# Kernel tuning notes

Measured on AMD Instinct MI355X. Metric: run time of the kernel, lower is better.

## Reference

```python
import jax, jax.numpy as jnp
import numpy as np

EMBED_DIM = 1024
NUM_HEADS = 16
PROJ_DIM = EMBED_DIM // NUM_HEADS


def setup_inputs() -> dict:
    key = jax.random.key(0)
    ks = jax.random.split(key, 11)
    B, S, D = 2, 2048, EMBED_DIM
    scale = 1.0 / np.sqrt(D)
    inp = {
        'q': jax.random.normal(ks[0], (B, S, D), jnp.float32),
        'k': jax.random.normal(ks[1], (B, S, D), jnp.float32),
        'v': jax.random.normal(ks[2], (B, S, D), jnp.float32),
        'Wq': jax.random.normal(ks[3], (D, D), jnp.float32) * scale,
        'bq': jnp.zeros((D,), jnp.float32),
        'Wk': jax.random.normal(ks[4], (D, D), jnp.float32) * scale,
        'bk': jnp.zeros((D,), jnp.float32),
        'Wv': jax.random.normal(ks[5], (D, D), jnp.float32) * scale,
        'bv': jnp.zeros((D,), jnp.float32),
        'Wo': jax.random.normal(ks[6], (D, D), jnp.float32) * scale,
        'bo': jnp.zeros((D,), jnp.float32),
        'use_causal_mask': 1,
    }
    return inp


def _split_heads(x, B):
    # [B, S, D] -> [B, H, S, Pd]
    return x.reshape(B, -1, NUM_HEADS, PROJ_DIM).transpose(0, 2, 1, 3)


def reference(q, k, v, Wq, bq, Wk, bk, Wv, bv, Wo, bo, use_causal_mask):
    B, S, D = q.shape
    qh = _split_heads(q @ Wq + bq, B)
    kh = _split_heads(k @ Wk + bk, B)
    vh = _split_heads(v @ Wv + bv, B)
    # scaled dot-product attention; scores [B, H, S, S]
    logits = jnp.einsum('bhqd,bhkd->bhqk', qh, kh) / jnp.sqrt(
        jnp.asarray(PROJ_DIM, jnp.float32))
    if use_causal_mask:
        # faithful to source: logits += log(tril * 1e-9 + 1e-9)
        tril = jnp.tril(jnp.ones((S, S), dtype=logits.dtype))
        logits = logits + jnp.log(tril * 1e-9 + 1e-9)
    attn = jax.nn.softmax(logits, axis=-1)
    out = jnp.einsum('bhqk,bhkd->bhqd', attn, vh)
    out = out.transpose(0, 2, 1, 3).reshape(B, S, D)
    return out @ Wo + bo
```

## Files before the change

kernel.cpp:

```cpp
#include <hip/hip_runtime.h>
#include <hip/hip_bf16.h>
#include <stdint.h>

#define EMBED 1024
#define NH    16
#define PD    64
#define BATCH 2
#define SEQ   2048

typedef unsigned short u16;
typedef __attribute__((ext_vector_type(8))) short bf16x8;
typedef __attribute__((ext_vector_type(4))) float f32x4;

#define WAITALL() __builtin_amdgcn_s_waitcnt(0)

__device__ __forceinline__ float b2f(u16 x) {
  unsigned u = ((unsigned)x) << 16;
  return __builtin_bit_cast(float, u);
}
__device__ __forceinline__ u16 cvtb(float x) {
  __bf16 h = (__bf16)x;
  return __builtin_bit_cast(u16, h);
}
__device__ __forceinline__ float loadIn(const void* p, size_t i, int isf32) {
  return isf32 ? ((const float*)p)[i] : b2f(((const u16*)p)[i]);
}
__device__ __forceinline__ void async16(const void* g, void* l) {
  __builtin_amdgcn_global_load_lds((const __attribute__((address_space(1))) void*)g,
                                   (__attribute__((address_space(3))) void*)l,
                                   16, 0, 0);
}
__device__ __forceinline__ int detect_f32(const void* q) {
  unsigned w0 = ((const unsigned*)q)[threadIdx.x & 63];
  unsigned e = (w0 >> 7) & 0xffu;
  unsigned long long m = __ballot(e >= 110 && e <= 135);
  return (__popcll(m) < 32) ? 1 : 0;
}

__global__ __launch_bounds__(256) void conv_fused(
    const void* q, const void* k, const void* v,
    const void* Wq, const void* Wk, const void* Wv, const void* Wo,
    u16* qb, u16* kb, u16* vb, u16* WT_all) {
  __shared__ float sh[64][65];
  const int isf32 = detect_f32(q);

  if (blockIdx.y < 3) {
    size_t i = ((size_t)blockIdx.x * 256 + threadIdx.x) * 8;
    const void* src = (blockIdx.y == 0) ? q : (blockIdx.y == 1) ? k : v;
    u16* dst = (blockIdx.y == 0) ? qb : (blockIdx.y == 1) ? kb : vb;
    u16 tmp[8];
    if (isf32) {
      const float* s = (const float*)src + i;
      float4 a = *(const float4*)s;
      float4 b = *(const float4*)(s + 4);
      tmp[0] = cvtb(a.x); tmp[1] = cvtb(a.y); tmp[2] = cvtb(a.z); tmp[3] = cvtb(a.w);
      tmp[4] = cvtb(b.x); tmp[5] = cvtb(b.y); tmp[6] = cvtb(b.z); tmp[7] = cvtb(b.w);
    } else {
      const uint4 r = *(const uint4*)((const u16*)src + i);
      *(uint4*)tmp = r;
    }
    *(uint4*)(dst + i) = *(uint4*)tmp;
    return;
  }

  if (blockIdx.x >= 1024) return;
  const int z = blockIdx.x >> 8;
  const int xy = blockIdx.x & 255;
  const int bx = xy & 15, by = xy >> 4;
  const void* W = (z == 0) ? Wq : (z == 1) ? Wk : (z == 2) ? Wv : Wo;
  u16* WT = WT_all + (size_t)z * EMBED * EMBED;
  int r0 = by * 64, c0 = bx * 64;
  int col = threadIdx.x & 63;
  int rb  = threadIdx.x >> 6;
#pragma unroll
  for (int i = 0; i < 16; i++) {
    int row = i * 4 + rb;
    sh[row][col] = loadIn(W, (size_t)(r0 + row) * EMBED + c0 + col, isf32);
  }
  __syncthreads();
#pragma unroll
  for (int i = 0; i < 16; i++) {
    int row = i * 4 + rb;
    WT[(size_t)(c0 + row) * EMBED + r0 + col] = cvtb(sh[col][row]);
  }
}

__device__ __forceinline__ void gemm_stage(const u16* __restrict__ A,
                                           const u16* __restrict__ Bt,
                                           int tm, int tn, int kt,
                                           u16* As, u16* Bs, int tid) {
#pragma unroll
  for (int i = 0; i < 4; i++) {
    int c = i * 256 + tid;
    int row = c >> 3;
    int col = ((c & 7) << 3) ^ ((row & 7) << 3);
    async16(A + (size_t)(tm + row) * EMBED + kt + col, As + c * 8);
    async16(Bt + (size_t)(tn + row) * EMBED + kt + col, Bs + c * 8);
  }
}

__device__ __forceinline__ void gemm_compute(const u16* As, const u16* Bs,
                                             int wm, int wn, int l15, int quad,
                                             int rbx, f32x4 acc[4][4]) {
#pragma unroll
  for (int ks = 0; ks < 64; ks += 32) {
    int ko = (ks + quad * 8) ^ rbx;
    bf16x8 af[4], bf[4];
#pragma unroll
    for (int mt = 0; mt < 4; mt++)
      af[mt] = *(const bf16x8*)(As + (wm + mt * 16 + l15) * 64 + ko);
#pragma unroll
    for (int nt = 0; nt < 4; nt++)
      bf[nt] = *(const bf16x8*)(Bs + (wn + nt * 16 + l15) * 64 + ko);
#pragma unroll
    for (int mt = 0; mt < 4; mt++)
#pragma unroll
      for (int nt = 0; nt < 4; nt++)
        acc[mt][nt] = __builtin_amdgcn_mfma_f32_16x16x32_bf16(
            af[mt], bf[nt], acc[mt][nt], 0, 0, 0);
  }
}

__global__ __launch_bounds__(256) void qkv_gemm(
    const u16* qb, const u16* kb, const u16* vb, const u16* wts,
    const void* bq, const void* bk, const void* bv,
    u16* Qh, u16* Kh, u16* Vt, const void* qorig) {
  __shared__ __align__(16) u16 lds[4 * 128 * 64];
  const int isf32 = detect_f32(qorig);

  const int lid = blockIdx.x + (blockIdx.y << 3) + (blockIdx.z << 8);
  const int mgrp = lid & 7;
  const int rest = lid >> 3;
  const int vx = rest & 7;
  const int vrest = rest >> 3;
  const int vm = vrest & 3;
  const int z = vrest >> 2;
  int tm = (mgrp * 4 + vm) * 128, tn = vx * 128;

  const u16* A = (z == 0) ? qb : (z == 1) ? kb : vb;
  const u16* Bt = wts + (size_t)z * EMBED * EMBED;
  const void* bias = (z == 0) ? bq : (z == 1) ? bk : bv;

  const int tid = threadIdx.x, lane = tid & 63, wv = tid >> 6;
  const int wm = (wv >> 1) * 64, wn = (wv & 1) * 64;
  const int l15 = lane & 15, quad = lane >> 4;
  const int rbx = (lane & 7) << 3;
  f32x4 acc[4][4];
  f32x4 zz = {0.f, 0.f, 0.f, 0.f};
#pragma unroll
  for (int i = 0; i < 4; i++)
#pragma unroll
    for (int j = 0; j < 4; j++) acc[i][j] = zz;

  gemm_stage(A, Bt, tm, tn, 0, lds, lds + 8192, tid);
  WAITALL();
  __syncthreads();
  for (int kt = 0; kt < EMBED; kt += 64) {
    const int cur = (kt >> 6) & 1;
    u16* curb = lds + cur * 16384;
    if (kt + 64 < EMBED)
      gemm_stage(A, Bt, tm, tn, kt + 64, lds + (cur ^ 1) * 16384,
                 lds + (cur ^ 1) * 16384 + 8192, tid);
    gemm_compute(curb, curb + 8192, wm, wn, l15, quad, rbx, acc);
    WAITALL();
    __syncthreads();
  }

  int rbase = tm + wm + (quad << 2);
  int cbase = tn + wn + l15;
  if (z < 2) {
    u16* dst = (z == 0) ? Qh : Kh;
#pragma unroll
    for (int mt = 0; mt < 4; mt++)
#pragma unroll
      for (int nt = 0; nt < 4; nt++) {
        int col = cbase + nt * 16;
        float bv_ = loadIn(bias, col, isf32);
        int h = col >> 6, p = col & 63;
#pragma unroll
        for (int j = 0; j < 4; j++) {
          int row = rbase + mt * 16 + j;
          int b = row >> 11, s = row & 2047;
          dst[(((size_t)(b * NH + h) * SEQ) + s) * PD + p] =
              cvtb(acc[mt][nt][j] + bv_);
        }
      }
  } else {
#pragma unroll
    for (int mt = 0; mt < 4; mt++)
#pragma unroll
      for (int nt = 0; nt < 4; nt++) {
        int col = cbase + nt * 16;
        float bv_ = loadIn(bias, col, isf32);
        int h = col >> 6, p = col & 63;
        int row0 = rbase + mt * 16;
        int b = row0 >> 11, s0 = row0 & 2047;
        int beta = s0 >> 5, w = s0 & 31;
        int pos = (beta << 5) + (((w >> 2) & 3) << 3) + ((w >> 4) << 2);
        ushort4 pk;
        pk.x = cvtb(acc[mt][nt][0] + bv_);
        pk.y = cvtb(acc[mt][nt][1] + bv_);
        pk.z = cvtb(acc[mt][nt][2] + bv_);
        pk.w = cvtb(acc[mt][nt][3] + bv_);
        *(ushort4*)(Vt + ((size_t)(b * NH + h) * PD + p) * SEQ + pos) = pk;
      }
  }
}

__global__ __launch_bounds__(256, 4) void attn(const u16* __restrict__ Qh,
                                               const u16* __restrict__ Kh,
                                               const u16* __restrict__ Vt,
                                               u16* __restrict__ O,
                                               const int* __restrict__ maskflag) {
  __shared__ __align__(16) u16 sh[5 * 64 * 64];
  u16* const Vbase = sh + 3 * 4096;
  u16* const Qs    = sh + 2 * 4096;

  const int lid = blockIdx.x + (blockIdx.y << 5);
  const int xcd = lid & 7, j = lid >> 3;
  const int bh = (xcd << 2) | (j & 3);
  const int qt = (j >> 2) * 64;

  const int tid = threadIdx.x, lane = tid & 63, wv = tid >> 6;
  const int qh = wv & 1;
  const int kh = wv >> 1;
  const int l15 = lane & 15, quad = lane >> 4;
  const int rbx = (lane & 7) << 3;
  const size_t head = (size_t)bh * SEQ * PD;
  const bool causal = (maskflag[0] != 0);
  const float C = 0.18033688011112042f;

  const int c0 = tid, c1 = 256 + tid;
  const int r0 = c0 >> 3, r1 = c1 >> 3;
  const int x0 = ((c0 & 7) << 3) ^ ((r0 & 7) << 3);
  const int x1 = ((c1 & 7) << 3) ^ ((r1 & 7) << 3);

  async16(Qh + head + (size_t)(qt + r0) * PD + x0, Qs + c0 * 8);
  async16(Qh + head + (size_t)(qt + r1) * PD + x1, Qs + c1 * 8);
  async16(Kh + head + (size_t)r0 * PD + x0, sh + c0 * 8);
  async16(Kh + head + (size_t)r1 * PD + x1, sh + c1 * 8);
  async16(Vt + head + (size_t)r0 * SEQ + x0, Vbase + c0 * 8);
  async16(Vt + head + (size_t)r1 * SEQ + x1, Vbase + c1 * 8);
  async16(Kh + head + (size_t)(64 + r0) * PD + x0, sh + 4096 + c0 * 8);
  async16(Kh + head + (size_t)(64 + r1) * PD + x1, sh + 4096 + c1 * 8);
  __syncthreads();

  bf16x8 qf[2][2];
#pragma unroll
  for (int ks = 0; ks < 2; ks++) {
    int ko = (ks * 32 + quad * 8) ^ rbx;
    qf[ks][0] = *(const bf16x8*)(Qs + (qh * 32 + l15) * 64 + ko);
    qf[ks][1] = *(const bf16x8*)(Qs + (qh * 32 + 16 + l15) * 64 + ko);
  }
  __syncthreads();

  float lacc[2] = {0.f, 0.f};
  f32x4 oacc[4][2];
  f32x4 z4 = {0.f, 0.f, 0.f, 0.f};
#pragma unroll
  for (int mt = 0; mt < 4; mt++)
#pragma unroll
    for (int qx = 0; qx < 2; qx++) oacc[mt][qx] = z4;

  const int qrow0 = qt + qh * 32 + l15;

  int b0 = 0, b1 = 1, b2 = 2;

  for (int t = 0; t < SEQ / 64; t++) {
    if (t == SEQ / 64 - 1) {
      asm volatile("s_waitcnt vmcnt(0)" ::: "memory");
    } else {
      asm volatile("s_waitcnt vmcnt(2)" ::: "memory");
    }
    __builtin_amdgcn_sched_barrier(0);
    __builtin_amdgcn_s_barrier();

    const int k0 = t * 64;
    if (t + 1 < SEQ / 64) {
      const int kn = k0 + 64;
      u16* Vn = Vbase + ((t + 1) & 1) * 4096;
      async16(Vt + head + (size_t)r0 * SEQ + kn + x0, Vn + c0 * 8);
      async16(Vt + head + (size_t)r1 * SEQ + kn + x1, Vn + c1 * 8);
    }
    if (t + 2 < SEQ / 64) {
      const int kn = k0 + 128;
      u16* Kn = sh + b2 * 4096;
      async16(Kh + head + (size_t)(kn + r0) * PD + x0, Kn + c0 * 8);
      async16(Kh + head + (size_t)(kn + r1) * PD + x1, Kn + c1 * 8);
    }
    const u16* Ksc = sh + b0 * 4096;
    const u16* Vsc = Vbase + (t & 1) * 4096;

    f32x4 st[2][2];
#pragma unroll
    for (int kx = 0; kx < 2; kx++)
#pragma unroll
      for (int qx = 0; qx < 2; qx++) st[kx][qx] = z4;
    __builtin_amdgcn_s_setprio(1);
#pragma unroll
    for (int ks = 0; ks < 2; ks++) {
      int ko = (ks * 32 + quad * 8) ^ rbx;
#pragma unroll
      for (int kx = 0; kx < 2; kx++) {
        bf16x8 kf = *(const bf16x8*)(Ksc + (kh * 32 + kx * 16 + l15) * 64 + ko);
        st[kx][0] = __builtin_amdgcn_mfma_f32_16x16x32_bf16(kf, qf[ks][0], st[kx][0], 0, 0, 0);
        st[kx][1] = __builtin_amdgcn_mfma_f32_16x16x32_bf16(kf, qf[ks][1], st[kx][1], 0, 0, 0);
      }
    }
    __builtin_amdgcn_s_setprio(0);

    const int mode = !causal ? 0 : (k0 > qt + 63 ? 2 : (k0 + 63 <= qt ? 0 : 1));
    const float ub = (mode == 2) ? -17.f : -16.f;
    unsigned pw[2][4];
#pragma unroll
    for (int kx = 0; kx < 2; kx++) {
#pragma unroll
      for (int qx = 0; qx < 2; qx++) {
        const int qrow = qrow0 + qx * 16;
        float p[4];
#pragma unroll
        for (int r = 0; r < 4; r++) {
          float bias = ub;
          if (mode == 1) {
            int kappa = k0 + kh * 32 + kx * 16 + 4 * quad + r;
            bias = (kappa > qrow) ? -17.f : -16.f;
          }
          p[r] = exp2f(fmaf(st[kx][qx][r], C, bias));
        }
        lacc[qx] += (p[0] + p[1]) + (p[2] + p[3]);
        pw[qx][kx * 2 + 0] =
            (unsigned)cvtb(p[0]) | ((unsigned)cvtb(p[1]) << 16);
        pw[qx][kx * 2 + 1] =
            (unsigned)cvtb(p[2]) | ((unsigned)cvtb(p[3]) << 16);
      }
    }

    __builtin_amdgcn_s_setprio(1);
    bf16x8 pf0 = __builtin_bit_cast(bf16x8,
        (uint4){pw[0][0], pw[0][1], pw[0][2], pw[0][3]});
    bf16x8 pf1 = __builtin_bit_cast(bf16x8,
        (uint4){pw[1][0], pw[1][1], pw[1][2], pw[1][3]});
#pragma unroll
    for (int mt = 0; mt < 4; mt++) {
      int row = mt * 16 + l15;
      int chunk = ((kh << 2) + quad) ^ (row & 7);
      bf16x8 vf = *(const bf16x8*)(Vsc + row * 64 + (chunk << 3));
      oacc[mt][0] = __builtin_amdgcn_mfma_f32_16x16x32_bf16(vf, pf0, oacc[mt][0], 0, 0, 0);
      oacc[mt][1] = __builtin_amdgcn_mfma_f32_16x16x32_bf16(vf, pf1, oacc[mt][1], 0, 0, 0);
    }
    __builtin_amdgcn_s_setprio(0);

    int tmp = b0; b0 = b1; b1 = b2; b2 = tmp;
  }

  __syncthreads();

#pragma unroll
  for (int qx = 0; qx < 2; qx++) {
    lacc[qx] += __shfl_xor(lacc[qx], 16, 64);
    lacc[qx] += __shfl_xor(lacc[qx], 32, 64);
  }

  float* red = (float*)sh;
  if (kh == 1) {
#pragma unroll
    for (int mt = 0; mt < 4; mt++)
#pragma unroll
      for (int qx = 0; qx < 2; qx++)
        *(f32x4*)(red + qh * 2048 + (mt * 2 + qx) * 256 + lane * 4) =
            oacc[mt][qx];
    red[4096 + qh * 128 + lane] = lacc[0];
    red[4096 + qh * 128 + 64 + lane] = lacc[1];
  }
  __syncthreads();
  if (kh == 0) {
    float l0 = lacc[0] + red[4096 + qh * 128 + lane];
    float l1 = lacc[1] + red[4096 + qh * 128 + 64 + lane];
    float inv[2] = {1.f / l0, 1.f / l1};
    const int b = bh >> 4, h = bh & 15;
#pragma unroll
    for (int mt = 0; mt < 4; mt++) {
#pragma unroll
      for (int qx = 0; qx < 2; qx++) {
        f32x4 o = oacc[mt][qx] +
                  *(const f32x4*)(red + qh * 2048 + (mt * 2 + qx) * 256 + lane * 4);
        int qrow = qrow0 + qx * 16;
        ushort4 w;
        w.x = cvtb(o[0] * inv[qx]);
        w.y = cvtb(o[1] * inv[qx]);
        w.z = cvtb(o[2] * inv[qx]);
        w.w = cvtb(o[3] * inv[qx]);
        *(ushort4*)(O + ((size_t)b * SEQ + qrow) * EMBED + h * PD + mt * 16 +
                    4 * quad) = w;
      }
    }
  }
}

__global__ __launch_bounds__(256) void out_gemm(const u16* __restrict__ Ob,
                                                const u16* __restrict__ WoT,
                                                const void* __restrict__ bo,
                                                void* __restrict__ out,
                                                const void* __restrict__ qorig) {
  __shared__ __align__(16) u16 lds[4 * 128 * 64];
  const int isf32 = detect_f32(qorig);

  const int lid = blockIdx.x + (blockIdx.y << 3);
  const int mgrp = lid & 7;
  const int vx = (lid >> 3) & 7;
  const int vm = lid >> 6;
  int tm = (mgrp * 4 + vm) * 128, tn = vx * 128;

  const int tid = threadIdx.x, lane = tid & 63, wv = tid >> 6;
  const int wm = (wv >> 1) * 64, wn = (wv & 1) * 64;
  const int l15 = lane & 15, quad = lane >> 4;
  const int rbx = (lane & 7) << 3;
  f32x4 acc[4][4];
  f32x4 zz = {0.f, 0.f, 0.f, 0.f};
#pragma unroll
  for (int i = 0; i < 4; i++)
#pragma unroll
    for (int j = 0; j < 4; j++) acc[i][j] = zz;

  gemm_stage(Ob, WoT, tm, tn, 0, lds, lds + 8192, tid);
  WAITALL();
  __syncthreads();
  for (int kt = 0; kt < EMBED; kt += 64) {
    const int cur = (kt >> 6) & 1;
    u16* curb = lds + cur * 16384;
    if (kt + 64 < EMBED)
      gemm_stage(Ob, WoT, tm, tn, kt + 64, lds + (cur ^ 1) * 16384,
                 lds + (cur ^ 1) * 16384 + 8192, tid);
    gemm_compute(curb, curb + 8192, wm, wn, l15, quad, rbx, acc);
    WAITALL();
    __syncthreads();
  }

  int rbase = tm + wm + (quad << 2);
  int cbase = tn + wn + l15;
#pragma unroll
  for (int mt = 0; mt < 4; mt++)
#pragma unroll
    for (int nt = 0; nt < 4; nt++) {
      int col = cbase + nt * 16;
      float bv_ = loadIn(bo, col, isf32);
#pragma unroll
      for (int j = 0; j < 4; j++) {
        int row = rbase + mt * 16 + j;
        float val = acc[mt][nt][j] + bv_;
        size_t off = (size_t)row * EMBED + col;
        if (isf32) ((float*)out)[off] = val;
        else       ((u16*)out)[off]   = cvtb(val);
      }
    }
}

extern "C" void kernel_launch(void* const* d_in, const int* in_sizes, int n_in,
                              void* d_out, int out_size, void* d_ws, size_t ws_size,
                              hipStream_t stream) {
  const void* q  = d_in[0];
  const void* k  = d_in[1];
  const void* v  = d_in[2];
  const void* Wq = d_in[3];
  const void* bq = d_in[4];
  const void* Wk = d_in[5];
  const void* bk = d_in[6];
  const void* Wv = d_in[7];
  const void* bv = d_in[8];
  const void* Wo = d_in[9];
  const void* bo = d_in[10];
  const int* msk = (const int*)d_in[11];

  char* ws = (char*)d_ws;
  u16*  qb    = (u16*)(ws + 64);
  u16*  kb    = qb + (size_t)4194304;
  u16*  vb    = kb + (size_t)4194304;
  u16*  WT    = vb + (size_t)4194304;
  u16*  Qh    = WT + (size_t)4194304;
  u16*  Kh    = Qh + (size_t)4194304;
  u16*  Vt    = Kh + (size_t)4194304;
  u16*  Ob    = Vt + (size_t)4194304;

  conv_fused<<<dim3(2048, 4), 256, 0, stream>>>(q, k, v, Wq, Wk, Wv, Wo,
                                                qb, kb, vb, WT);
  qkv_gemm<<<dim3(8, 32, 3), 256, 0, stream>>>(qb, kb, vb, WT, bq, bk, bv,
                                               Qh, Kh, Vt, q);
  attn<<<dim3(32, 32), 256, 0, stream>>>(Qh, Kh, Vt, Ob, msk);
  out_gemm<<<dim3(8, 32), 256, 0, stream>>>(Ob, WT + (size_t)3 * 1048576,
                                            bo, d_out, q);
}
```

Measured before the change: 268.0 us.

## Enlarge QKV GEMM tiles to 256x256 with 512-thread blocks

```diff
diff --git a/kernel.cpp b/kernel.cpp
--- a/kernel.cpp
+++ b/kernel.cpp
@@ -121,57 +121,85 @@
   }
 }
 
-__global__ __launch_bounds__(256) void qkv_gemm(
+__global__ __launch_bounds__(512, 2) void qkv_gemm(
     const u16* qb, const u16* kb, const u16* vb, const u16* wts,
     const void* bq, const void* bk, const void* bv,
     u16* Qh, u16* Kh, u16* Vt, const void* qorig) {
-  __shared__ __align__(16) u16 lds[4 * 128 * 64];
+  __shared__ __align__(16) u16 lds[4 * 256 * 64];
   const int isf32 = detect_f32(qorig);
 
-  const int lid = blockIdx.x + (blockIdx.y << 3) + (blockIdx.z << 8);
-  const int mgrp = lid & 7;
-  const int rest = lid >> 3;
-  const int vx = rest & 7;
-  const int vrest = rest >> 3;
-  const int vm = vrest & 3;
-  const int z = vrest >> 2;
-  int tm = (mgrp * 4 + vm) * 128, tn = vx * 128;
+  const int lid = blockIdx.x;
+  const int mhi = lid & 7;
+  const int mlo = (lid >> 3) & 1;
+  const int vx = (lid >> 4) & 3;
+  const int z = lid >> 6;
+  const int vm = mhi * 2 + mlo;
+  const int tm = vm * 256, tn = vx * 256;
 
   const u16* A = (z == 0) ? qb : (z == 1) ? kb : vb;
   const u16* Bt = wts + (size_t)z * EMBED * EMBED;
   const void* bias = (z == 0) ? bq : (z == 1) ? bk : bv;
 
   const int tid = threadIdx.x, lane = tid & 63, wv = tid >> 6;
-  const int wm = (wv >> 1) * 64, wn = (wv & 1) * 64;
+  const int wm = (wv >> 2) * 128, wn = (wv & 3) * 64;
   const int l15 = lane & 15, quad = lane >> 4;
   const int rbx = (lane & 7) << 3;
-  f32x4 acc[4][4];
+
+  f32x4 acc[8][4];
   f32x4 zz = {0.f, 0.f, 0.f, 0.f};
 #pragma unroll
-  for (int i = 0; i < 4; i++)
+  for (int i = 0; i < 8; i++)
 #pragma unroll
     for (int j = 0; j < 4; j++) acc[i][j] = zz;
 
-  gemm_stage(A, Bt, tm, tn, 0, lds, lds + 8192, tid);
+#define QKV_STAGE(kt_, As_, Bs_)                                              \
+  {                                                                           \
+    _Pragma("unroll") for (int i = 0; i < 4; i++) {                           \
+      int c = i * 512 + tid;                                                  \
+      int row = c >> 3;                                                       \
+      int col = ((c & 7) << 3) ^ ((row & 7) << 3);                            \
+      async16(A + (size_t)(tm + row) * EMBED + (kt_) + col, (As_) + c * 8);   \
+      async16(Bt + (size_t)(tn + row) * EMBED + (kt_) + col, (Bs_) + c * 8);  \
+    }                                                                         \
+  }
+
+  QKV_STAGE(0, lds, lds + 16384);
   WAITALL();
   __syncthreads();
   for (int kt = 0; kt < EMBED; kt += 64) {
     const int cur = (kt >> 6) & 1;
-    u16* curb = lds + cur * 16384;
+    const u16* Asc = lds + cur * 32768;
+    const u16* Bsc = Asc + 16384;
     if (kt + 64 < EMBED)
-      gemm_stage(A, Bt, tm, tn, kt + 64, lds + (cur ^ 1) * 16384,
-                 lds + (cur ^ 1) * 16384 + 8192, tid);
-    gemm_compute(curb, curb + 8192, wm, wn, l15, quad, rbx, acc);
+      QKV_STAGE(kt + 64, lds + (cur ^ 1) * 32768, lds + (cur ^ 1) * 32768 + 16384);
+#pragma unroll
+    for (int ks = 0; ks < 64; ks += 32) {
+      int ko = (ks + quad * 8) ^ rbx;
+      bf16x8 af[8], bf[4];
+#pragma unroll
+      for (int mt = 0; mt < 8; mt++)
+        af[mt] = *(const bf16x8*)(Asc + (wm + mt * 16 + l15) * 64 + ko);
+#pragma unroll
+      for (int nt = 0; nt < 4; nt++)
+        bf[nt] = *(const bf16x8*)(Bsc + (wn + nt * 16 + l15) * 64 + ko);
+#pragma unroll
+      for (int mt = 0; mt < 8; mt++)
+#pragma unroll
+        for (int nt = 0; nt < 4; nt++)
+          acc[mt][nt] = __builtin_amdgcn_mfma_f32_16x16x32_bf16(
+              af[mt], bf[nt], acc[mt][nt], 0, 0, 0);
+    }
     WAITALL();
     __syncthreads();
   }
+#undef QKV_STAGE
 
   int rbase = tm + wm + (quad << 2);
   int cbase = tn + wn + l15;
   if (z < 2) {
     u16* dst = (z == 0) ? Qh : Kh;
 #pragma unroll
-    for (int mt = 0; mt < 4; mt++)
+    for (int mt = 0; mt < 8; mt++)
 #pragma unroll
       for (int nt = 0; nt < 4; nt++) {
         int col = cbase + nt * 16;
@@ -187,7 +215,7 @@
       }
   } else {
 #pragma unroll
-    for (int mt = 0; mt < 4; mt++)
+    for (int mt = 0; mt < 8; mt++)
 #pragma unroll
       for (int nt = 0; nt < 4; nt++) {
         int col = cbase + nt * 16;
@@ -483,8 +511,8 @@
 
   conv_fused<<<dim3(2048, 4), 256, 0, stream>>>(q, k, v, Wq, Wk, Wv, Wo,
                                                 qb, kb, vb, WT);
-  qkv_gemm<<<dim3(8, 32, 3), 256, 0, stream>>>(qb, kb, vb, WT, bq, bk, bv,
-                                               Qh, Kh, Vt, q);
+  qkv_gemm<<<dim3(192), 512, 0, stream>>>(qb, kb, vb, WT, bq, bk, bv,
+                                          Qh, Kh, Vt, q);
   attn<<<dim3(32, 32), 256, 0, stream>>>(Qh, Kh, Vt, Ob, msk);
   out_gemm<<<dim3(8, 32), 256, 0, stream>>>(Ob, WT + (size_t)3 * 1048576,
                                             bo, d_out, q);
```

Measured after the change: 258.0 us. 1.04x faster.
